# Optimization experiments

Hardware: AMD Instinct MI355X
Metric: run time of the kernel (lower is better)

## Reference

```python
import jax, jax.numpy as jnp
import numpy as np

B, C, H, W = 4, 96, 64, 64
CS = 8                      # chunk size
DN = 2 * C                  # d_inner (expand=2)
N = 16                      # d_state
K = 4                       # scan directions
DT_R = (C + 15) // 16       # dt_rank = ceil(d_model/16)
EPS = 1e-5


def _ln(x, g, b):
    m = x.mean(-1, keepdims=True)
    v = ((x - m) ** 2).mean(-1, keepdims=True)
    return (x - m) / jnp.sqrt(v + EPS) * g + b


def _selective_scan(xs, delta, A, Bs, Cs, D):
    # xs, delta: (Bc, K, Dn, L); Bs, Cs: (Bc, K, N, L); A: (K, Dn, N); D: (K, Dn)
    Bc, Kk, Dn, L = xs.shape
    uT = xs.transpose(3, 0, 1, 2)       # (L, Bc, K, Dn)
    dT = delta.transpose(3, 0, 1, 2)
    BT = Bs.transpose(3, 0, 1, 2)       # (L, Bc, K, N)
    CT = Cs.transpose(3, 0, 1, 2)

    def step(h, inp):
        u_l, d_l, B_l, C_l = inp
        dA = jnp.exp(d_l[..., None] * A)                       # (Bc,K,Dn,N)
        h = h * dA + (d_l * u_l)[..., None] * B_l[:, :, None, :]
        y = jnp.einsum('bkdn,bkn->bkd', h, C_l)
        return h, y

    h0 = jnp.zeros((Bc, Kk, Dn, A.shape[-1]), xs.dtype)
    _, ys = jax.lax.scan(step, h0, (uT, dT, BT, CT))           # ys: (L,Bc,K,Dn)
    ys = ys.transpose(1, 2, 3, 0)                              # (Bc,K,Dn,L)
    return ys + D[None, :, :, None] * xs


def _ss2d(xh, in_proj_w, conv_w, conv_b, x_proj_w, dt_w, dt_b,
          A_logs, Ds, outnorm_g, outnorm_b, out_proj_w):
    # xh: (Bc, Hc, Wc, C)
    Bc, Hc, Wc, _ = xh.shape
    L = Hc * Wc
    xz = xh @ in_proj_w                                        # (Bc,Hc,Wc,2*Dn)
    xc, z = jnp.split(xz, 2, axis=-1)
    xc = xc.transpose(0, 3, 1, 2)                              # (Bc,Dn,Hc,Wc)
    xc = jax.lax.conv_general_dilated(xc, conv_w, (1, 1), ((1, 1), (1, 1)),
                                      feature_group_count=DN)
    xc = jax.nn.silu(xc + conv_b[None, :, None, None])
    x0 = xc.reshape(Bc, DN, L)                                 # HW order
    x1 = xc.transpose(0, 1, 3, 2).reshape(Bc, DN, L)           # WH order
    xs = jnp.stack([x0, x1, x0[:, :, ::-1], x1[:, :, ::-1]], axis=1)  # (Bc,4,Dn,L)
    x_dbl = jnp.einsum('bkdl,kcd->bkcl', xs, x_proj_w)         # (Bc,4,DT_R+2N,L)
    dts = x_dbl[:, :, :DT_R]
    Bs = x_dbl[:, :, DT_R:DT_R + N]
    Cs = x_dbl[:, :, DT_R + N:]
    dts = jnp.einsum('bkrl,kdr->bkdl', dts, dt_w)
    delta = jax.nn.softplus(dts + dt_b[None, :, :, None])      # (Bc,4,Dn,L)
    A = -jnp.exp(A_logs).reshape(K, DN, N)
    ys = _selective_scan(xs, delta, A, Bs, Cs, Ds.reshape(K, DN))
    y0 = ys[:, 0]
    y1 = ys[:, 1].reshape(Bc, DN, Wc, Hc).transpose(0, 1, 3, 2).reshape(Bc, DN, L)
    y2 = ys[:, 2, :, ::-1]
    y3 = ys[:, 3, :, ::-1].reshape(Bc, DN, Wc, Hc).transpose(0, 1, 3, 2).reshape(Bc, DN, L)
    y = (y0 + y1 + y2 + y3).transpose(0, 2, 1)                 # (Bc,L,Dn)
    y = _ln(y, outnorm_g, outnorm_b).reshape(Bc, Hc, Wc, DN)
    y = y * jax.nn.silu(z)
    return y @ out_proj_w                                      # (Bc,Hc,Wc,C)


def reference(x, gamma, beta, alpha, ln1_g, ln1_b, in_proj_w, conv_w, conv_b,
              x_proj_w, dt_w, dt_b, A_logs, Ds, outnorm_g, outnorm_b, out_proj_w):
    Bb, Cc, Hh, Ww = x.shape
    # StateNorm: per (b, c) over spatial dims, unbiased=False
    mean = x.mean(axis=(2, 3), keepdims=True)
    var = ((x - mean) ** 2).mean(axis=(2, 3), keepdims=True)
    x_norm = (x - mean) / jnp.sqrt(var + EPS)
    x_norm = gamma[None, :, None, None] * x_norm + beta[None, :, None, None]
    x_act = jax.nn.silu(x_norm)                 # act_quant with bits=32 is identity
    hn, wn = Hh // CS, Ww // CS
    # chunk: b c (hn cs)(wn cs) -> (b hn wn) c cs cs
    xc = x_act.reshape(Bb, Cc, hn, CS, wn, CS).transpose(0, 2, 4, 1, 3, 5)
    xc = xc.reshape(Bb * hn * wn, Cc, CS, CS)
    # VSSBlock: h + SS2D(LN(h)) in BHWC (drop_path = identity at inference)
    h = xc.transpose(0, 2, 3, 1)                # (Bc, cs, cs, C)
    h = h + _ss2d(_ln(h, ln1_g, ln1_b), in_proj_w, conv_w, conv_b, x_proj_w,
                  dt_w, dt_b, A_logs, Ds, outnorm_g, outnorm_b, out_proj_w)
    xv = h.transpose(0, 3, 1, 2)                # back to BCHW
    # unchunk
    xv = xv.reshape(Bb, hn, wn, Cc, CS, CS).transpose(0, 3, 1, 4, 2, 5)
    xv = xv.reshape(Bb, Cc, Hh, Ww)
    return x + alpha * xv


def setup_inputs() -> dict:
    key = jax.random.key(0)
    ks = jax.random.split(key, 12)
    s = 0.02
    inp = {
        'x': jax.random.normal(ks[0], (B, C, H, W), jnp.float32),
        'gamma': jnp.ones((C,), jnp.float32),
        'beta': jnp.zeros((C,), jnp.float32),
        'alpha': jnp.float32(0.5),
        'ln1_g': jnp.ones((C,), jnp.float32),
        'ln1_b': jnp.zeros((C,), jnp.float32),
        'in_proj_w': jax.random.normal(ks[1], (C, 2 * DN), jnp.float32) / np.sqrt(C),
        'conv_w': jax.random.normal(ks[2], (DN, 1, 3, 3), jnp.float32) / 3.0,
        'conv_b': jnp.zeros((DN,), jnp.float32),
        'x_proj_w': jax.random.normal(ks[3], (K, DT_R + 2 * N, DN), jnp.float32) / np.sqrt(DN),
        'dt_w': jax.random.normal(ks[4], (K, DN, DT_R), jnp.float32) * (DT_R ** -0.5),
        'dt_b': jnp.full((K, DN), -4.6, jnp.float32) + s * jax.random.normal(ks[5], (K, DN), jnp.float32),
        'A_logs': jnp.log(jnp.broadcast_to(jnp.arange(1, N + 1, dtype=jnp.float32), (K * DN, N))).copy(),
        'Ds': jnp.ones((K * DN,), jnp.float32),
        'outnorm_g': jnp.ones((DN,), jnp.float32),
        'outnorm_b': jnp.zeros((DN,), jnp.float32),
        'out_proj_w': jax.random.normal(ks[6], (DN, C), jnp.float32) / np.sqrt(DN),
    }
    return inp
```

## Files before the change

### kernel.cpp

```cpp
#include <hip/hip_runtime.h>
#include <math.h>

__device__ __forceinline__ float siluf_(float x) {
    return x / (1.f + __expf(-x));
}

__device__ __forceinline__ int sperm(int k, int l) {
    int t = (k & 1) ? (((l & 7) << 3) | (l >> 3)) : l;
    return (k & 2) ? (63 - t) : t;
}

__device__ __forceinline__ unsigned int f2bf(float f) {
    unsigned int u = __float_as_uint(f);
    return (u + 0x7FFFu + ((u >> 16) & 1u)) >> 16;
}
__device__ __forceinline__ float bf2f(unsigned int h) {
    return __uint_as_float(h << 16);
}
__device__ __forceinline__ unsigned int packbf(float lo, float hi) {
    return f2bf(lo) | (f2bf(hi) << 16);
}

__global__ void k1a_stats(const float* __restrict__ x, float* __restrict__ stats) {
    int bc = blockIdx.x;
    const float* xp = x + (size_t)bc * 4096;
    float s = 0.f, sq = 0.f;
    for (int i = threadIdx.x; i < 4096; i += 256) {
        float v = xp[i]; s += v; sq += v * v;
    }
    __shared__ float rs[256], rq[256];
    rs[threadIdx.x] = s; rq[threadIdx.x] = sq;
    __syncthreads();
    for (int off = 128; off > 0; off >>= 1) {
        if (threadIdx.x < off) {
            rs[threadIdx.x] += rs[threadIdx.x + off];
            rq[threadIdx.x] += rq[threadIdx.x + off];
        }
        __syncthreads();
    }
    if (threadIdx.x == 0) {
        float m = rs[0] * (1.f / 4096.f);
        float v = rq[0] * (1.f / 4096.f) - m * m;
        stats[bc] = m;
        stats[384 + bc] = rsqrtf(v + 1e-5f);
    }
}

__global__ __launch_bounds__(256) void kA(
        const float* __restrict__ x, const float* __restrict__ stats,
        const float* __restrict__ gamma, const float* __restrict__ beta,
        const float* __restrict__ ln1_g, const float* __restrict__ ln1_b,
        const float* __restrict__ Win,
        float* __restrict__ xcg_all,
        unsigned int* __restrict__ zg_b) {
    int blk = blockIdx.x;
    int xcd = blk & 7, j = blk >> 3;
    int chunk = xcd * 32 + (j >> 2), cg = j & 3;
    int b = chunk >> 6, chh = (chunk >> 3) & 7, chw = chunk & 7;
    __shared__ float hs[64 * 97];
    int t = threadIdx.x;
    for (int i = t; i < 6144; i += 256) {
        int c = i >> 6, pos = i & 63;
        int bc = b * 96 + c;
        int hh = chh * 8 + (pos >> 3), ww = chw * 8 + (pos & 7);
        float v = x[(((size_t)bc) * 64 + hh) * 64 + ww];
        float xn = (v - stats[bc]) * stats[384 + bc] * gamma[c] + beta[c];
        hs[pos * 97 + c] = siluf_(xn);
    }
    __syncthreads();
    {
        int p = t >> 2, o = t & 3;
        float s = 0.f, sq = 0.f;
        #pragma unroll
        for (int jj = 0; jj < 24; jj++) { float v = hs[p * 97 + o + 4 * jj]; s += v; sq += v * v; }
        s += __shfl_xor(s, 1); sq += __shfl_xor(sq, 1);
        s += __shfl_xor(s, 2); sq += __shfl_xor(sq, 2);
        float m = s * (1.f / 96.f);
        float rinv = rsqrtf(sq * (1.f / 96.f) - m * m + 1e-5f);
        #pragma unroll
        for (int jj = 0; jj < 24; jj++) {
            int c = o + 4 * jj;
            hs[p * 97 + c] = (hs[p * 97 + c] - m) * rinv * ln1_g[c] + ln1_b[c];
        }
    }
    __syncthreads();
    int p = t & 63;
    int wv = __builtin_amdgcn_readfirstlane(t >> 6);
    int jbase = cg * 96 + wv * 24;
    float acc[24];
    #pragma unroll
    for (int i = 0; i < 24; i++) acc[i] = 0.f;
    for (int c = 0; c < 96; c++) {
        float u = hs[p * 97 + c];
        const float* w = Win + c * 384 + jbase;
        #pragma unroll
        for (int i = 0; i < 24; i++) acc[i] = fmaf(u, w[i], acc[i]);
    }
    if (jbase < 192) {
        float* o_ = xcg_all + (size_t)chunk * 12288 + jbase * 64 + p;
        #pragma unroll
        for (int i = 0; i < 24; i++) o_[i * 64] = acc[i];
    } else {
        int i2base = (jbase - 192) >> 1;
        unsigned int* o_ = zg_b + (size_t)chunk * 6144 + i2base * 64 + p;
        #pragma unroll
        for (int i = 0; i < 12; i++) o_[i * 64] = packbf(acc[2 * i], acc[2 * i + 1]);
    }
}

__global__ __launch_bounds__(256) void kB(
        const float* __restrict__ xcg_all, const float* __restrict__ conv_w,
        const float* __restrict__ conv_b, float* __restrict__ x0T_all) {
    int blk = blockIdx.x;
    int xcd = blk & 7, j = blk >> 3;
    int chunk = xcd * 32 + (j >> 2), dg = j & 3;
    int dbase = dg * 48;
    __shared__ float tile[48 * 65];
    int t = threadIdx.x;
    const float* in = xcg_all + (size_t)chunk * 12288 + dbase * 64;
    for (int i = t; i < 3072; i += 256) tile[(i >> 6) * 65 + (i & 63)] = in[i];
    __syncthreads();
    float* o = x0T_all + (size_t)chunk * 12288;
    for (int s = 0; s < 12; s++) {
        int idx = s * 256 + t;
        int l = idx / 48, dl = idx - l * 48;
        int r = l >> 3, cc = l & 7;
        int d = dbase + dl;
        float acc = conv_b[d];
        #pragma unroll
        for (int dh = 0; dh < 3; dh++) {
            int rr = r + dh - 1;
            if (rr < 0 || rr > 7) continue;
            #pragma unroll
            for (int dw = 0; dw < 3; dw++) {
                int cw = cc + dw - 1;
                if (cw < 0 || cw > 7) continue;
                acc = fmaf(tile[dl * 65 + rr * 8 + cw], conv_w[d * 9 + dh * 3 + dw], acc);
            }
        }
        o[l * 192 + d] = siluf_(acc);
    }
}

__global__ __launch_bounds__(384, 6) void kD(
        const float* __restrict__ x0T_all, const float* __restrict__ xpw,
        const float* __restrict__ dtw, const float* __restrict__ dtb,
        const float* __restrict__ A_logs, const float* __restrict__ Ds,
        unsigned int* __restrict__ yk01,
        unsigned int* __restrict__ yk23) {
    int blk = blockIdx.x;
    int xcd = blk & 7, j = blk >> 3;
    int chunk = xcd * 32 + (j >> 2);
    int k = j & 3;
    __shared__ float pT[64 * 40];
    int t = threadIdx.x;
    const float* xbase = x0T_all + (size_t)chunk * 12288;

    {
        int l = t & 63;
        int wv6 = __builtin_amdgcn_readfirstlane(t >> 6);
        int cbase = wv6 * 7;
        float acc[7];
        #pragma unroll
        for (int i = 0; i < 7; i++) acc[i] = 0.f;
        const float* xl = xbase + l * 192;
        const float* wb = xpw + (size_t)k * 38 * 192;
        for (int dd = 0; dd < 192; dd += 4) {
            float4 u4 = *(const float4*)(xl + dd);
            #pragma unroll
            for (int ci = 0; ci < 7; ci++) {
                int c = cbase + ci;
                if (c < 38) {
                    float4 w4 = *(const float4*)(wb + c * 192 + dd);
                    acc[ci] = fmaf(u4.x, w4.x, acc[ci]);
                    acc[ci] = fmaf(u4.y, w4.y, acc[ci]);
                    acc[ci] = fmaf(u4.z, w4.z, acc[ci]);
                    acc[ci] = fmaf(u4.w, w4.w, acc[ci]);
                }
            }
        }
        #pragma unroll
        for (int ci = 0; ci < 7; ci++) {
            int c = cbase + ci;
            if (c < 38) {
                int slot = c + (c >= 6 ? 2 : 0);
                pT[l * 40 + slot] = acc[ci];
            }
        }
    }
    __syncthreads();

    {
        int d = t >> 1, h = t & 1;
        int gd = k * 192 + d;
        float w6[6];
        #pragma unroll
        for (int r = 0; r < 6; r++) w6[r] = dtw[gd * 6 + r];
        float bias = dtb[gd];
        float Dd_eff = h ? 0.f : Ds[gd];
        float a0 = -__expf(A_logs[gd * 16]);
        float a8[8];
        #pragma unroll
        for (int n = 0; n < 8; n++) a8[n] = -__expf(A_logs[gd * 16 + 8 * h + n]);
        bool pw = true;
        #pragma unroll
        for (int n = 0; n < 8; n++) {
            float tgt = (float)(8 * h + n + 1) * a0;
            pw = pw && (fabsf(a8[n] - tgt) <= 1e-4f * fabsf(tgt) + 1e-6f);
        }
        bool a0m1 = (a0 == -1.0f);
        float c0 = a0 * (float)(8 * h + 1);
        float hst[8];
        #pragma unroll
        for (int n = 0; n < 8; n++) hst[n] = 0.f;
        unsigned int* yb = (k < 2 ? yk01 : yk23) + (size_t)(k & 1) * 1572864
                           + (size_t)chunk * 6144;
        int hb = 8 * h;

        if (__all(pw && a0m1)) {
            for (int g8 = 0; g8 < 8; ++g8) {
                float u8[8];
                #pragma unroll
                for (int i = 0; i < 8; i++)
                    u8[i] = xbase[sperm(k, g8 * 8 + i) * 192 + d];
                #pragma unroll
                for (int i = 0; i < 8; i += 2) {
                    int sl0 = sperm(k, g8 * 8 + i);
                    int sl1 = sperm(k, g8 * 8 + i + 1);
                    const float* row0 = pT + sl0 * 40;
                    const float* row1 = pT + sl1 * 40;
                    float4 rA0 = *(const float4*)(row0);
                    float2 rB0 = *(const float2*)(row0 + 4);
                    float4 b00 = *(const float4*)(row0 + 8 + hb);
                    float4 b01 = *(const float4*)(row0 + 12 + hb);
                    float4 c00 = *(const float4*)(row0 + 24 + hb);
                    float4 c01 = *(const float4*)(row0 + 28 + hb);
                    float4 rA1 = *(const float4*)(row1);
                    float2 rB1 = *(const float2*)(row1 + 4);
                    float4 b10 = *(const float4*)(row1 + 8 + hb);
                    float4 b11 = *(const float4*)(row1 + 12 + hb);
                    float4 c10 = *(const float4*)(row1 + 24 + hb);
                    float4 c11 = *(const float4*)(row1 + 28 + hb);
                    float dp0 = bias, dp1 = bias;
                    dp0 = fmaf(rA0.x, w6[0], dp0); dp1 = fmaf(rA1.x, w6[0], dp1);
                    dp0 = fmaf(rA0.y, w6[1], dp0); dp1 = fmaf(rA1.y, w6[1], dp1);
                    dp0 = fmaf(rA0.z, w6[2], dp0); dp1 = fmaf(rA1.z, w6[2], dp1);
                    dp0 = fmaf(rA0.w, w6[3], dp0); dp1 = fmaf(rA1.w, w6[3], dp1);
                    dp0 = fmaf(rB0.x, w6[4], dp0); dp1 = fmaf(rB1.x, w6[4], dp1);
                    dp0 = fmaf(rB0.y, w6[5], dp0); dp1 = fmaf(rB1.y, w6[5], dp1);
                    float ex0 = __expf(dp0), ex1 = __expf(dp1);
                    float delta0 = (dp0 > 20.f) ? dp0 : __logf(1.f + ex0);
                    float delta1 = (dp1 > 20.f) ? dp1 : __logf(1.f + ex1);
                    float e10 = __builtin_amdgcn_rcpf(1.f + ex0);
                    float e11 = __builtin_amdgcn_rcpf(1.f + ex1);
                    float du0 = delta0 * u8[i];
                    float du1 = delta1 * u8[i + 1];
                    float e20 = e10 * e10, e40 = e20 * e20, e80 = e40 * e40;
                    float ebm0 = e80 * e10;
                    float eb0 = h ? ebm0 : e10;
                    float p0 = eb0,       p1 = eb0 * e10, p2 = eb0 * e20, p3 = p1 * e20;
                    float p4 = eb0 * e40, p5 = p1 * e40,  p6 = p2 * e40,  p7 = p3 * e40;
                    float e21 = e11 * e11, e41 = e21 * e21, e81 = e41 * e41;
                    float ebm1 = e81 * e11;
                    float eb1 = h ? ebm1 : e11;
                    float q0 = eb1,       q1 = eb1 * e11, q2 = eb1 * e21, q3 = q1 * e21;
                    float q4 = eb1 * e41, q5 = q1 * e41,  q6 = q2 * e41,  q7 = q3 * e41;
                    float ya, yb_;
                    hst[0] = fmaf(hst[0], p0, du0 * b00.x); ya  = hst[0] * c00.x;
                    hst[1] = fmaf(hst[1], p1, du0 * b00.y); yb_ = hst[1] * c00.y;
                    hst[2] = fmaf(hst[2], p2, du0 * b00.z); ya  = fmaf(hst[2], c00.z, ya);
                    hst[3] = fmaf(hst[3], p3, du0 * b00.w); yb_ = fmaf(hst[3], c00.w, yb_);
                    hst[4] = fmaf(hst[4], p4, du0 * b01.x); ya  = fmaf(hst[4], c01.x, ya);
                    hst[5] = fmaf(hst[5], p5, du0 * b01.y); yb_ = fmaf(hst[5], c01.y, yb_);
                    hst[6] = fmaf(hst[6], p6, du0 * b01.z); ya  = fmaf(hst[6], c01.z, ya);
                    hst[7] = fmaf(hst[7], p7, du0 * b01.w); yb_ = fmaf(hst[7], c01.w, yb_);
                    float yp0 = fmaf(Dd_eff, u8[i], ya + yb_);
                    float yf0 = yp0 + __shfl_xor(yp0, 1);
                    float yo0 = __shfl_xor(yf0, 2);
                    if ((t & 3) == 0) yb[sl0 * 96 + (d >> 1)] = packbf(yf0, yo0);
                    hst[0] = fmaf(hst[0], q0, du1 * b10.x); ya  = hst[0] * c10.x;
                    hst[1] = fmaf(hst[1], q1, du1 * b10.y); yb_ = hst[1] * c10.y;
                    hst[2] = fmaf(hst[2], q2, du1 * b10.z); ya  = fmaf(hst[2], c10.z, ya);
                    hst[3] = fmaf(hst[3], q3, du1 * b10.w); yb_ = fmaf(hst[3], c10.w, yb_);
                    hst[4] = fmaf(hst[4], q4, du1 * b11.x); ya  = fmaf(hst[4], c11.x, ya);
                    hst[5] = fmaf(hst[5], q5, du1 * b11.y); yb_ = fmaf(hst[5], c11.y, yb_);
                    hst[6] = fmaf(hst[6], q6, du1 * b11.z); ya  = fmaf(hst[6], c11.z, ya);
                    hst[7] = fmaf(hst[7], q7, du1 * b11.w); yb_ = fmaf(hst[7], c11.w, yb_);
                    float yp1 = fmaf(Dd_eff, u8[i + 1], ya + yb_);
                    float yf1 = yp1 + __shfl_xor(yp1, 1);
                    float yo1 = __shfl_xor(yf1, 2);
                    if ((t & 3) == 0) yb[sl1 * 96 + (d >> 1)] = packbf(yf1, yo1);
                }
            }
        } else if (__all(pw)) {
            for (int g8 = 0; g8 < 8; ++g8) {
                float u8[8];
                #pragma unroll
                for (int i = 0; i < 8; i++)
                    u8[i] = xbase[sperm(k, g8 * 8 + i) * 192 + d];
                #pragma unroll
                for (int i = 0; i < 8; i++) {
                    int sl = sperm(k, g8 * 8 + i);
                    const float* row = pT + sl * 40;
                    float4 rA = *(const float4*)(row);
                    float2 rB = *(const float2*)(row + 4);
                    float dp = bias;
                    dp = fmaf(rA.x, w6[0], dp); dp = fmaf(rA.y, w6[1], dp);
                    dp = fmaf(rA.z, w6[2], dp); dp = fmaf(rA.w, w6[3], dp);
                    dp = fmaf(rB.x, w6[4], dp); dp = fmaf(rB.y, w6[5], dp);
                    float delta = (dp > 20.f) ? dp : __logf(1.f + __expf(dp));
                    float du = delta * u8[i];
                    float e1 = __expf(delta * a0);
                    float eb = __expf(delta * c0);
                    float e2 = e1 * e1, e4 = e2 * e2;
                    float p0 = eb,      p1 = eb * e1, p2 = eb * e2, p3 = p1 * e2;
                    float p4 = p0 * e4, p5 = p1 * e4, p6 = p2 * e4, p7 = p3 * e4;
                    float4 bq0 = *(const float4*)(row + 8 + hb);
                    float4 bq1 = *(const float4*)(row + 12 + hb);
                    float4 cq0 = *(const float4*)(row + 24 + hb);
                    float4 cq1 = *(const float4*)(row + 28 + hb);
                    float y0, y1;
                    hst[0] = fmaf(hst[0], p0, du * bq0.x); y0 = hst[0] * cq0.x;
                    hst[1] = fmaf(hst[1], p1, du * bq0.y); y1 = hst[1] * cq0.y;
                    hst[2] = fmaf(hst[2], p2, du * bq0.z); y0 = fmaf(hst[2], cq0.z, y0);
                    hst[3] = fmaf(hst[3], p3, du * bq0.w); y1 = fmaf(hst[3], cq0.w, y1);
                    hst[4] = fmaf(hst[4], p4, du * bq1.x); y0 = fmaf(hst[4], cq1.x, y0);
                    hst[5] = fmaf(hst[5], p5, du * bq1.y); y1 = fmaf(hst[5], cq1.y, y1);
                    hst[6] = fmaf(hst[6], p6, du * bq1.z); y0 = fmaf(hst[6], cq1.z, y0);
                    hst[7] = fmaf(hst[7], p7, du * bq1.w); y1 = fmaf(hst[7], cq1.w, y1);
                    float yp = fmaf(Dd_eff, u8[i], y0 + y1);
                    float yfull = yp + __shfl_xor(yp, 1);
                    float yo2 = __shfl_xor(yfull, 2);
                    if ((t & 3) == 0) yb[sl * 96 + (d >> 1)] = packbf(yfull, yo2);
                }
            }
        } else {
            for (int l = 0; l < 64; l++) {
                int sl = sperm(k, l);
                float u = xbase[sl * 192 + d];
                const float* row = pT + sl * 40;
                float dp = bias;
                #pragma unroll
                for (int r = 0; r < 6; r++) dp = fmaf(row[r], w6[r], dp);
                float delta = (dp > 20.f) ? dp : __logf(1.f + __expf(dp));
                float du = delta * u;
                float yp = 0.f;
                #pragma unroll
                for (int n = 0; n < 8; n++) {
                    float e = __expf(delta * a8[n]);
                    hst[n] = fmaf(hst[n], e, du * row[8 + hb + n]);
                    yp = fmaf(hst[n], row[24 + hb + n], yp);
                }
                yp = fmaf(Dd_eff, u, yp);
                float yfull = yp + __shfl_xor(yp, 1);
                float yo2 = __shfl_xor(yfull, 2);
                if ((t & 3) == 0) yb[sl * 96 + (d >> 1)] = packbf(yfull, yo2);
            }
        }
    }
}

__global__ __launch_bounds__(256) void kE(
        const unsigned int* __restrict__ yk01, const unsigned int* __restrict__ yk23,
        const unsigned int* __restrict__ zg_b,
        const float* __restrict__ og, const float* __restrict__ ob,
        float* __restrict__ g_all) {
    int blk = blockIdx.x;
    int xcd = blk & 7, j = blk >> 3;
    int chunk = xcd * 32 + (j >> 1), half = j & 1;
    int t = threadIdx.x;
    int p = half * 32 + (t >> 3), o = t & 7;
    int par = o & 1;
    size_t rb = (size_t)chunk * 6144 + p * 96;
    const unsigned int* r0 = yk01 + rb;
    const unsigned int* r1 = yk01 + 1572864 + rb;
    const unsigned int* r2 = yk23 + rb;
    const unsigned int* r3 = yk23 + 1572864 + rb;
    float ys[24];
    float s = 0.f, sq = 0.f;
    #pragma unroll
    for (int jj = 0; jj < 24; jj++) {
        int i = o + 8 * jj;
        int wi = i >> 1;
        int sh = par ? 16 : 0;
        float v = bf2f((r0[wi] >> sh) & 0xFFFFu) + bf2f((r1[wi] >> sh) & 0xFFFFu)
                + bf2f((r2[wi] >> sh) & 0xFFFFu) + bf2f((r3[wi] >> sh) & 0xFFFFu);
        ys[jj] = v; s += v; sq += v * v;
    }
    s += __shfl_xor(s, 1); sq += __shfl_xor(sq, 1);
    s += __shfl_xor(s, 2); sq += __shfl_xor(sq, 2);
    s += __shfl_xor(s, 4); sq += __shfl_xor(sq, 4);
    float m = s * (1.f / 192.f);
    float rinv = rsqrtf(sq * (1.f / 192.f) - m * m + 1e-5f);
    const unsigned int* z = zg_b + (size_t)chunk * 6144;
    float* g = g_all + (size_t)chunk * 12288;
    #pragma unroll
    for (int jj = 0; jj < 24; jj++) {
        int i = o + 8 * jj;
        float ln = (ys[jj] - m) * rinv * og[i] + ob[i];
        unsigned int zw = z[(i >> 1) * 64 + p];
        float zv = bf2f(par ? (zw >> 16) : (zw & 0xFFFFu));
        g[i * 64 + p] = ln * siluf_(zv);
    }
}

__global__ __launch_bounds__(256) void kF(
        const float* __restrict__ g_all, const float* __restrict__ Wout,
        const float* __restrict__ x, const float* __restrict__ stats,
        const float* __restrict__ gamma, const float* __restrict__ beta,
        const float* __restrict__ alpha, float* __restrict__ out) {
    int blk = blockIdx.x;
    int xcd = blk & 7, j = blk >> 3;
    int chunk = xcd * 32 + (j >> 2), cgf = j & 3;
    int b = chunk >> 6, chh = (chunk >> 3) & 7, chw = chunk & 7;
    int t = threadIdx.x;
    int p = t & 63;
    int wv = __builtin_amdgcn_readfirstlane(t >> 6);
    int cbase = cgf * 24 + wv * 6;
    float acc[6];
    #pragma unroll
    for (int i = 0; i < 6; i++) acc[i] = 0.f;
    const float* g = g_all + (size_t)chunk * 12288;
    for (int dd = 0; dd < 192; dd++) {
        float u = g[dd * 64 + p];
        const float* w = Wout + dd * 96 + cbase;
        #pragma unroll
        for (int i = 0; i < 6; i++) acc[i] = fmaf(u, w[i], acc[i]);
    }
    float al = alpha[0];
    int hh = chh * 8 + (p >> 3), ww = chw * 8 + (p & 7);
    #pragma unroll
    for (int i = 0; i < 6; i++) {
        int c = cbase + i;
        int bc = b * 96 + c;
        size_t gi = (((size_t)bc) * 64 + hh) * 64 + ww;
        float xv = x[gi];
        float xn = (xv - stats[bc]) * stats[384 + bc] * gamma[c] + beta[c];
        out[gi] = xv + al * (siluf_(xn) + acc[i]);
    }
}

extern "C" void kernel_launch(void* const* d_in, const int* in_sizes, int n_in,
                              void* d_out, int out_size, void* d_ws, size_t ws_size,
                              hipStream_t stream) {
    const float* x        = (const float*)d_in[0];
    const float* gamma    = (const float*)d_in[1];
    const float* beta     = (const float*)d_in[2];
    const float* alpha    = (const float*)d_in[3];
    const float* ln1_g    = (const float*)d_in[4];
    const float* ln1_b    = (const float*)d_in[5];
    const float* in_proj  = (const float*)d_in[6];
    const float* conv_w   = (const float*)d_in[7];
    const float* conv_b   = (const float*)d_in[8];
    const float* x_proj   = (const float*)d_in[9];
    const float* dt_w     = (const float*)d_in[10];
    const float* dt_b     = (const float*)d_in[11];
    const float* A_logs   = (const float*)d_in[12];
    const float* Ds       = (const float*)d_in[13];
    const float* onorm_g  = (const float*)d_in[14];
    const float* onorm_b  = (const float*)d_in[15];
    const float* out_proj = (const float*)d_in[16];
    float* out = (float*)d_out;

    float* ws    = (float*)d_ws;
    float* stats = ws;
    float* xcg   = ws + 768;
    float* x0T   = xcg + 3145728;
    unsigned int* zg_b = (unsigned int*)(x0T + 3145728);
    unsigned int* yk23 = zg_b + 1572864;
    unsigned int* yk01 = (unsigned int*)xcg;
    float* gbuf  = x0T;

    hipLaunchKernelGGL(k1a_stats, dim3(384), dim3(256), 0, stream, x, stats);
    hipLaunchKernelGGL(kA, dim3(1024), dim3(256), 0, stream,
                       x, stats, gamma, beta, ln1_g, ln1_b, in_proj, xcg, zg_b);
    hipLaunchKernelGGL(kB, dim3(1024), dim3(256), 0, stream,
                       xcg, conv_w, conv_b, x0T);
    hipLaunchKernelGGL(kD, dim3(1024), dim3(384), 0, stream,
                       x0T, x_proj, dt_w, dt_b, A_logs, Ds, yk01, yk23);
    hipLaunchKernelGGL(kE, dim3(512), dim3(256), 0, stream,
                       yk01, yk23, zg_b, onorm_g, onorm_b, gbuf);
    hipLaunchKernelGGL(kF, dim3(1024), dim3(256), 0, stream,
                       gbuf, out_proj, x, stats, gamma, beta, alpha, out);
}
```

Before: 203.3 us.

## Fuse in-proj with depthwise conv and out-norm with out-proj via LDS

```diff
diff --git a/kernel.cpp b/kernel.cpp
--- a/kernel.cpp
+++ b/kernel.cpp
@@ -46,18 +46,20 @@
     }
 }
 
-__global__ __launch_bounds__(256) void kA(
+__global__ __launch_bounds__(256) void kAB(
         const float* __restrict__ x, const float* __restrict__ stats,
         const float* __restrict__ gamma, const float* __restrict__ beta,
         const float* __restrict__ ln1_g, const float* __restrict__ ln1_b,
         const float* __restrict__ Win,
-        float* __restrict__ xcg_all,
+        const float* __restrict__ conv_w, const float* __restrict__ conv_b,
+        float* __restrict__ x0T_all,
         unsigned int* __restrict__ zg_b) {
     int blk = blockIdx.x;
     int xcd = blk & 7, j = blk >> 3;
-    int chunk = xcd * 32 + (j >> 2), cg = j & 3;
+    int chunk = xcd * 32 + (j >> 1), cg = j & 1;
     int b = chunk >> 6, chh = (chunk >> 3) & 7, chw = chunk & 7;
     __shared__ float hs[64 * 97];
+    __shared__ float xc[96 * 65];
     int t = threadIdx.x;
     for (int i = t; i < 6144; i += 256) {
         int c = i >> 6, pos = i & 63;
@@ -84,61 +86,52 @@
         }
     }
     __syncthreads();
-    int p = t & 63;
-    int wv = __builtin_amdgcn_readfirstlane(t >> 6);
-    int jbase = cg * 96 + wv * 24;
-    float acc[24];
-    #pragma unroll
-    for (int i = 0; i < 24; i++) acc[i] = 0.f;
-    for (int c = 0; c < 96; c++) {
-        float u = hs[p * 97 + c];
-        const float* w = Win + c * 384 + jbase;
-        #pragma unroll
-        for (int i = 0; i < 24; i++) acc[i] = fmaf(u, w[i], acc[i]);
-    }
-    if (jbase < 192) {
-        float* o_ = xcg_all + (size_t)chunk * 12288 + jbase * 64 + p;
-        #pragma unroll
-        for (int i = 0; i < 24; i++) o_[i * 64] = acc[i];
-    } else {
-        int i2base = (jbase - 192) >> 1;
+    {
+        int p = t & 63;
+        int wv = __builtin_amdgcn_readfirstlane(t >> 6);
+        int jc = cg * 96 + wv * 24;
+        int jz = 192 + jc;
+        float acc[48];
+        #pragma unroll
+        for (int i = 0; i < 48; i++) acc[i] = 0.f;
+        for (int c = 0; c < 96; c++) {
+            float u = hs[p * 97 + c];
+            const float* w = Win + c * 384;
+            #pragma unroll
+            for (int i = 0; i < 24; i++) acc[i] = fmaf(u, w[jc + i], acc[i]);
+            #pragma unroll
+            for (int i = 0; i < 24; i++) acc[24 + i] = fmaf(u, w[jz + i], acc[24 + i]);
+        }
+        #pragma unroll
+        for (int i = 0; i < 24; i++) xc[(wv * 24 + i) * 65 + p] = acc[i];
+        int i2base = cg * 48 + wv * 12;
         unsigned int* o_ = zg_b + (size_t)chunk * 6144 + i2base * 64 + p;
         #pragma unroll
-        for (int i = 0; i < 12; i++) o_[i * 64] = packbf(acc[2 * i], acc[2 * i + 1]);
-    }
-}
-
-__global__ __launch_bounds__(256) void kB(
-        const float* __restrict__ xcg_all, const float* __restrict__ conv_w,
-        const float* __restrict__ conv_b, float* __restrict__ x0T_all) {
-    int blk = blockIdx.x;
-    int xcd = blk & 7, j = blk >> 3;
-    int chunk = xcd * 32 + (j >> 2), dg = j & 3;
-    int dbase = dg * 48;
-    __shared__ float tile[48 * 65];
-    int t = threadIdx.x;
-    const float* in = xcg_all + (size_t)chunk * 12288 + dbase * 64;
-    for (int i = t; i < 3072; i += 256) tile[(i >> 6) * 65 + (i & 63)] = in[i];
-    __syncthreads();
-    float* o = x0T_all + (size_t)chunk * 12288;
-    for (int s = 0; s < 12; s++) {
-        int idx = s * 256 + t;
-        int l = idx / 48, dl = idx - l * 48;
-        int r = l >> 3, cc = l & 7;
-        int d = dbase + dl;
-        float acc = conv_b[d];
-        #pragma unroll
-        for (int dh = 0; dh < 3; dh++) {
-            int rr = r + dh - 1;
-            if (rr < 0 || rr > 7) continue;
+        for (int m2 = 0; m2 < 12; m2++)
+            o_[m2 * 64] = packbf(acc[24 + 2 * m2], acc[24 + 2 * m2 + 1]);
+    }
+    __syncthreads();
+    {
+        float* x0o = x0T_all + (size_t)chunk * 12288 + cg * 96;
+        for (int s = 0; s < 24; s++) {
+            int idx = s * 256 + t;
+            int l = idx / 96, dl = idx - l * 96;
+            int d = cg * 96 + dl;
+            int r = l >> 3, cc = l & 7;
+            float acc = conv_b[d];
             #pragma unroll
-            for (int dw = 0; dw < 3; dw++) {
-                int cw = cc + dw - 1;
-                if (cw < 0 || cw > 7) continue;
-                acc = fmaf(tile[dl * 65 + rr * 8 + cw], conv_w[d * 9 + dh * 3 + dw], acc);
-            }
-        }
-        o[l * 192 + d] = siluf_(acc);
+            for (int dh = 0; dh < 3; dh++) {
+                int rr = r + dh - 1;
+                if (rr < 0 || rr > 7) continue;
+                #pragma unroll
+                for (int dw = 0; dw < 3; dw++) {
+                    int cw = cc + dw - 1;
+                    if (cw < 0 || cw > 7) continue;
+                    acc = fmaf(xc[dl * 65 + rr * 8 + cw], conv_w[d * 9 + dh * 3 + dw], acc);
+                }
+            }
+            x0o[l * 192 + dl] = siluf_(acc);
+        }
     }
 }
 
@@ -360,83 +353,79 @@
     }
 }
 
-__global__ __launch_bounds__(256) void kE(
+__global__ __launch_bounds__(256) void kEF(
         const unsigned int* __restrict__ yk01, const unsigned int* __restrict__ yk23,
         const unsigned int* __restrict__ zg_b,
         const float* __restrict__ og, const float* __restrict__ ob,
-        float* __restrict__ g_all) {
-    int blk = blockIdx.x;
-    int xcd = blk & 7, j = blk >> 3;
-    int chunk = xcd * 32 + (j >> 1), half = j & 1;
-    int t = threadIdx.x;
-    int p = half * 32 + (t >> 3), o = t & 7;
-    int par = o & 1;
-    size_t rb = (size_t)chunk * 6144 + p * 96;
-    const unsigned int* r0 = yk01 + rb;
-    const unsigned int* r1 = yk01 + 1572864 + rb;
-    const unsigned int* r2 = yk23 + rb;
-    const unsigned int* r3 = yk23 + 1572864 + rb;
-    float ys[24];
-    float s = 0.f, sq = 0.f;
-    #pragma unroll
-    for (int jj = 0; jj < 24; jj++) {
-        int i = o + 8 * jj;
-        int wi = i >> 1;
-        int sh = par ? 16 : 0;
-        float v = bf2f((r0[wi] >> sh) & 0xFFFFu) + bf2f((r1[wi] >> sh) & 0xFFFFu)
-                + bf2f((r2[wi] >> sh) & 0xFFFFu) + bf2f((r3[wi] >> sh) & 0xFFFFu);
-        ys[jj] = v; s += v; sq += v * v;
-    }
-    s += __shfl_xor(s, 1); sq += __shfl_xor(sq, 1);
-    s += __shfl_xor(s, 2); sq += __shfl_xor(sq, 2);
-    s += __shfl_xor(s, 4); sq += __shfl_xor(sq, 4);
-    float m = s * (1.f / 192.f);
-    float rinv = rsqrtf(sq * (1.f / 192.f) - m * m + 1e-5f);
-    const unsigned int* z = zg_b + (size_t)chunk * 6144;
-    float* g = g_all + (size_t)chunk * 12288;
-    #pragma unroll
-    for (int jj = 0; jj < 24; jj++) {
-        int i = o + 8 * jj;
-        float ln = (ys[jj] - m) * rinv * og[i] + ob[i];
-        unsigned int zw = z[(i >> 1) * 64 + p];
-        float zv = bf2f(par ? (zw >> 16) : (zw & 0xFFFFu));
-        g[i * 64 + p] = ln * siluf_(zv);
-    }
-}
-
-__global__ __launch_bounds__(256) void kF(
-        const float* __restrict__ g_all, const float* __restrict__ Wout,
+        const float* __restrict__ Wout,
         const float* __restrict__ x, const float* __restrict__ stats,
         const float* __restrict__ gamma, const float* __restrict__ beta,
         const float* __restrict__ alpha, float* __restrict__ out) {
     int blk = blockIdx.x;
     int xcd = blk & 7, j = blk >> 3;
-    int chunk = xcd * 32 + (j >> 2), cgf = j & 3;
+    int chunk = xcd * 32 + (j >> 1), cgf = j & 1;
     int b = chunk >> 6, chh = (chunk >> 3) & 7, chw = chunk & 7;
+    __shared__ float gs[64 * 193];
     int t = threadIdx.x;
-    int p = t & 63;
-    int wv = __builtin_amdgcn_readfirstlane(t >> 6);
-    int cbase = cgf * 24 + wv * 6;
-    float acc[6];
-    #pragma unroll
-    for (int i = 0; i < 6; i++) acc[i] = 0.f;
-    const float* g = g_all + (size_t)chunk * 12288;
-    for (int dd = 0; dd < 192; dd++) {
-        float u = g[dd * 64 + p];
-        const float* w = Wout + dd * 96 + cbase;
-        #pragma unroll
-        for (int i = 0; i < 6; i++) acc[i] = fmaf(u, w[i], acc[i]);
-    }
-    float al = alpha[0];
-    int hh = chh * 8 + (p >> 3), ww = chw * 8 + (p & 7);
-    #pragma unroll
-    for (int i = 0; i < 6; i++) {
-        int c = cbase + i;
-        int bc = b * 96 + c;
-        size_t gi = (((size_t)bc) * 64 + hh) * 64 + ww;
-        float xv = x[gi];
-        float xn = (xv - stats[bc]) * stats[384 + bc] * gamma[c] + beta[c];
-        out[gi] = xv + al * (siluf_(xn) + acc[i]);
+    for (int half = 0; half < 2; half++) {
+        int p = half * 32 + (t >> 3), o = t & 7;
+        int par = o & 1;
+        size_t rb = (size_t)chunk * 6144 + p * 96;
+        const unsigned int* r0 = yk01 + rb;
+        const unsigned int* r1 = yk01 + 1572864 + rb;
+        const unsigned int* r2 = yk23 + rb;
+        const unsigned int* r3 = yk23 + 1572864 + rb;
+        float ys[24];
+        float s = 0.f, sq = 0.f;
+        #pragma unroll
+        for (int jj = 0; jj < 24; jj++) {
+            int i = o + 8 * jj;
+            int wi = i >> 1;
+            int sh = par ? 16 : 0;
+            float v = bf2f((r0[wi] >> sh) & 0xFFFFu) + bf2f((r1[wi] >> sh) & 0xFFFFu)
+                    + bf2f((r2[wi] >> sh) & 0xFFFFu) + bf2f((r3[wi] >> sh) & 0xFFFFu);
+            ys[jj] = v; s += v; sq += v * v;
+        }
+        s += __shfl_xor(s, 1); sq += __shfl_xor(sq, 1);
+        s += __shfl_xor(s, 2); sq += __shfl_xor(sq, 2);
+        s += __shfl_xor(s, 4); sq += __shfl_xor(sq, 4);
+        float m = s * (1.f / 192.f);
+        float rinv = rsqrtf(sq * (1.f / 192.f) - m * m + 1e-5f);
+        const unsigned int* z = zg_b + (size_t)chunk * 6144;
+        #pragma unroll
+        for (int jj = 0; jj < 24; jj++) {
+            int i = o + 8 * jj;
+            float ln = (ys[jj] - m) * rinv * og[i] + ob[i];
+            unsigned int zw = z[(i >> 1) * 64 + p];
+            float zv = bf2f(par ? (zw >> 16) : (zw & 0xFFFFu));
+            gs[p * 193 + i] = ln * siluf_(zv);
+        }
+    }
+    __syncthreads();
+    {
+        int p = t & 63;
+        int wv = __builtin_amdgcn_readfirstlane(t >> 6);
+        int cbase = cgf * 48 + wv * 12;
+        float acc[12];
+        #pragma unroll
+        for (int i = 0; i < 12; i++) acc[i] = 0.f;
+        for (int dd = 0; dd < 192; dd++) {
+            float u = gs[p * 193 + dd];
+            const float* w = Wout + dd * 96 + cbase;
+            #pragma unroll
+            for (int i = 0; i < 12; i++) acc[i] = fmaf(u, w[i], acc[i]);
+        }
+        float al = alpha[0];
+        int hh = chh * 8 + (p >> 3), ww = chw * 8 + (p & 7);
+        #pragma unroll
+        for (int i = 0; i < 12; i++) {
+            int c = cbase + i;
+            int bc = b * 96 + c;
+            size_t gi = (((size_t)bc) * 64 + hh) * 64 + ww;
+            float xv = x[gi];
+            float xn = (xv - stats[bc]) * stats[384 + bc] * gamma[c] + beta[c];
+            out[gi] = xv + al * (siluf_(xn) + acc[i]);
+        }
     }
 }
 
@@ -464,22 +453,18 @@
 
     float* ws    = (float*)d_ws;
     float* stats = ws;
-    float* xcg   = ws + 768;
-    float* x0T   = xcg + 3145728;
+    float* x0T   = ws + 768;
     unsigned int* zg_b = (unsigned int*)(x0T + 3145728);
-    unsigned int* yk23 = zg_b + 1572864;
-    unsigned int* yk01 = (unsigned int*)xcg;
-    float* gbuf  = x0T;
+    unsigned int* yk01 = zg_b + 1572864;
+    unsigned int* yk23 = yk01 + 3145728;
 
     hipLaunchKernelGGL(k1a_stats, dim3(384), dim3(256), 0, stream, x, stats);
-    hipLaunchKernelGGL(kA, dim3(1024), dim3(256), 0, stream,
-                       x, stats, gamma, beta, ln1_g, ln1_b, in_proj, xcg, zg_b);
-    hipLaunchKernelGGL(kB, dim3(1024), dim3(256), 0, stream,
-                       xcg, conv_w, conv_b, x0T);
+    hipLaunchKernelGGL(kAB, dim3(512), dim3(256), 0, stream,
+                       x, stats, gamma, beta, ln1_g, ln1_b, in_proj,
+                       conv_w, conv_b, x0T, zg_b);
     hipLaunchKernelGGL(kD, dim3(1024), dim3(384), 0, stream,
                        x0T, x_proj, dt_w, dt_b, A_logs, Ds, yk01, yk23);
-    hipLaunchKernelGGL(kE, dim3(512), dim3(256), 0, stream,
-                       yk01, yk23, zg_b, onorm_g, onorm_b, gbuf);
-    hipLaunchKernelGGL(kF, dim3(1024), dim3(256), 0, stream,
-                       gbuf, out_proj, x, stats, gamma, beta, alpha, out);
-}
+    hipLaunchKernelGGL(kEF, dim3(512), dim3(256), 0, stream,
+                       yk01, yk23, zg_b, onorm_g, onorm_b, out_proj,
+                       x, stats, gamma, beta, alpha, out);
+}
```

Result: no change. 202.3 us (-0.5%).
